# Optimization experiments

Hardware: AMD Instinct MI355X
Metric: run time of the kernel (lower is better)

The kernel has to match this reference:

```python
import jax, jax.numpy as jnp
import numpy as np

D_MODEL = 1024
N_HEADS = 16
D_HEAD = D_MODEL // N_HEADS
B, S = 2, 2048


def setup_inputs() -> dict:
    key = jax.random.key(0)
    ks = jax.random.split(key, 7)
    query = jax.random.normal(ks[0], (B, S, D_MODEL), dtype=jnp.float32)
    k_in = jax.random.normal(ks[1], (B, S, D_MODEL), dtype=jnp.float32)
    v_in = jax.random.normal(ks[2], (B, S, D_MODEL), dtype=jnp.float32)
    # causal mask: True = attend allowed (torch code keeps where mask != 0)
    mask = jnp.tril(jnp.ones((S, S), dtype=bool))
    scale = 1.0 / np.sqrt(D_MODEL)
    Wq = jax.random.normal(ks[3], (D_MODEL, D_MODEL), dtype=jnp.float32) * scale
    Wk = jax.random.normal(ks[4], (D_MODEL, D_MODEL), dtype=jnp.float32) * scale
    Wv = jax.random.normal(ks[5], (D_MODEL, D_MODEL), dtype=jnp.float32) * scale
    Wo = jax.random.normal(ks[6], (D_MODEL, D_MODEL), dtype=jnp.float32) * scale
    return {"query": query, "key": k_in, "value": v_in, "mask": mask,
            "Wq": Wq, "Wk": Wk, "Wv": Wv, "Wo": Wo}


def reference(query, key, value, mask, Wq, Wk, Wv, Wo):
    b, sq, d = query.shape
    # bias-free linear: x @ W.T (torch nn.Linear convention)
    q = (query @ Wq.T).reshape(b, sq, N_HEADS, D_HEAD).transpose(0, 2, 1, 3)  # b h s d
    k = (key @ Wk.T).reshape(b, -1, N_HEADS, D_HEAD).transpose(0, 2, 1, 3)
    v = (value @ Wv.T).reshape(b, -1, N_HEADS, D_HEAD).transpose(0, 2, 1, 3)
    scores = jnp.einsum('bhqd,bhkd->bhqk', q, k) / jnp.sqrt(jnp.float32(D_HEAD))
    scores = jnp.where(mask[None, None, :, :], scores, jnp.float32(-1e9))
    attn = jax.nn.softmax(scores, axis=-1)
    # dropout is identity in eval mode
    ctx = jnp.einsum('bhqk,bhkd->bhqd', attn, v)
    ctx = ctx.transpose(0, 2, 1, 3).reshape(b, sq, d)
    return ctx @ Wo.T
```

## Files before the change

### kernel.cpp

```cpp
#include <hip/hip_runtime.h>
#include <hip/hip_bf16.h>
#include <cstdint>


typedef unsigned short u16;
typedef u16 u16x4 __attribute__((ext_vector_type(4)));
typedef u16 u16x8 __attribute__((ext_vector_type(8)));
typedef unsigned u32x2 __attribute__((ext_vector_type(2)));
typedef unsigned u32x4 __attribute__((ext_vector_type(4)));
typedef __bf16 bf16x8 __attribute__((ext_vector_type(8)));
typedef float f32x4 __attribute__((ext_vector_type(4)));

#define S_LEN 2048
#define DM 1024
#define NH 16
#define DH 64
#define BATCH 2
#define MTOT (BATCH*S_LEN)

__device__ __forceinline__ u16 f2bf(float f) {
  union { float f; unsigned u; } v; v.f = f;
  unsigned r = v.u + 0x7FFFu + ((v.u >> 16) & 1u);
  return (u16)(r >> 16);
}

__device__ __forceinline__ f32x4 mfma16(u16x8 a, u16x8 b, f32x4 c) {
  return __builtin_amdgcn_mfma_f32_16x16x32_bf16(
      __builtin_bit_cast(bf16x8, a), __builtin_bit_cast(bf16x8, b), c, 0, 0, 0);
}
__device__ __forceinline__ unsigned cvtpk_bf16(float lo, float hi) {
  unsigned r;
  asm("v_cvt_pk_bf16_f32 %0, %1, %2" : "=v"(r) : "v"(lo), "v"(hi));
  return r;
}
__device__ __forceinline__ void gload16(const u16* g, u16* l) {
  __builtin_amdgcn_global_load_lds(
      (const __attribute__((address_space(1))) unsigned int*)g,
      (__attribute__((address_space(3))) unsigned int*)l, 16, 0, 0);
}

__global__ __launch_bounds__(256) void cvt_kernel(
    const float* __restrict__ s0, const float* __restrict__ s1,
    const float* __restrict__ s2, const float* __restrict__ s3,
    u16* __restrict__ d0, u16* __restrict__ d1,
    u16* __restrict__ d2, u16* __restrict__ d3) {
  const int y = blockIdx.y;
  const float* s = (y == 0) ? s0 : (y == 1) ? s1 : (y == 2) ? s2 : s3;
  u16* d       = (y == 0) ? d0 : (y == 1) ? d1 : (y == 2) ? d2 : d3;
  int i = (blockIdx.x * 256 + threadIdx.x) * 4;
  f32x4 v = *(const f32x4*)&s[i];
  u16x4 o;
  o[0] = f2bf(v[0]); o[1] = f2bf(v[1]); o[2] = f2bf(v[2]); o[3] = f2bf(v[3]);
  *(u16x4*)&d[i] = o;
}

#define BM 128
#define BN 128
#define BKK 32

template<int MODE, bool AF32>
__device__ __forceinline__ void gemm_core(const void* __restrict__ Av,
                                          const u16* __restrict__ Bw,
                                          void* __restrict__ Cv,
                                          int K, float scale,
                                          int bx, int by, u16* smem) {
  const int BUFSZ = AF32 ? 12288 : 8192;
  const int AOFF  = AF32 ? 8192  : 4096;
  const u16* A16 = (const u16*)Av;
  const float* A32 = (const float*)Av;
  const int tid  = threadIdx.x;
  const int lane = tid & 63, w = tid >> 6;
  const int g = lane >> 4, r16 = lane & 15;
  const int wm = w >> 1, wn = w & 1;
  const int rowBase = by * BM;
  const int colBase = bx * BN;
  f32x4 acc[4][4] = {};

  const int srowB = lane >> 2;
  const int skcB  = (lane & 3) * 8;
  const u16* gB[2]; int oB[2];
#pragma unroll
  for (int j = 0; j < 2; j++) {
    const int c = w * 2 + j;
    gB[j] = &Bw[(size_t)(colBase + c * 16 + srowB) * K + skcB];
    oB[j] = c * 512;
  }
  const u16* gA16[2]; int oA16[2];
  const float* gA32[4]; int oA32[4];
  if constexpr (AF32) {
    const int srow8 = lane >> 3;
    const int scF   = ((lane & 7) ^ srow8) * 4;
#pragma unroll
    for (int j = 0; j < 4; j++) {
      const int rb = w * 32 + j * 8;
      gA32[j] = &A32[(size_t)(rowBase + rb + srow8) * K + scF];
      oA32[j] = rb * 32;
    }
  } else {
#pragma unroll
    for (int j = 0; j < 2; j++) {
      const int c = w * 2 + j;
      gA16[j] = &A16[(size_t)(rowBase + c * 16 + srowB) * K + skcB];
      oA16[j] = c * 512;
    }
  }

  const int NT = K / BKK;
  {
    u16* base = smem;
    if constexpr (AF32) {
      float* a32 = (float*)base;
#pragma unroll
      for (int j = 0; j < 4; j++) gload16((const u16*)gA32[j], (u16*)(a32 + oA32[j]));
    } else {
#pragma unroll
      for (int j = 0; j < 2; j++) gload16(gA16[j], base + oA16[j]);
    }
#pragma unroll
    for (int j = 0; j < 2; j++) gload16(gB[j], base + AOFF + oB[j]);
  }
  int cur = 0;
  for (int t = 0; t < NT; ++t) {
    __syncthreads();
    if (t + 1 < NT) {
      const int k0 = (t + 1) * BKK;
      u16* base = smem + (cur ^ 1) * BUFSZ;
      if constexpr (AF32) {
        float* a32 = (float*)base;
#pragma unroll
        for (int j = 0; j < 4; j++) gload16((const u16*)(gA32[j] + k0), (u16*)(a32 + oA32[j]));
      } else {
#pragma unroll
        for (int j = 0; j < 2; j++) gload16(gA16[j] + k0, base + oA16[j]);
      }
#pragma unroll
      for (int j = 0; j < 2; j++) gload16(gB[j] + k0, base + AOFF + oB[j]);
    }
    u16* As = smem + cur * BUFSZ;
    u16* Bs = As + AOFF;
    float* As32 = (float*)As;
    u16x8 af[4], bfv[4];
    if constexpr (AF32) {
      const int rx = r16 & 7;
#pragma unroll
      for (int i = 0; i < 4; i++) {
        const int base_ = (wm * 64 + i * 16 + r16) * 32;
        f32x4 a0 = *(const f32x4*)&As32[base_ + (((g * 2)     ^ rx) * 4)];
        f32x4 a1 = *(const f32x4*)&As32[base_ + (((g * 2 + 1) ^ rx) * 4)];
        u32x4 wv = {cvtpk_bf16(a0[0], a0[1]), cvtpk_bf16(a0[2], a0[3]),
                    cvtpk_bf16(a1[0], a1[1]), cvtpk_bf16(a1[2], a1[3])};
        af[i] = __builtin_bit_cast(u16x8, wv);
      }
    } else {
#pragma unroll
      for (int i = 0; i < 4; i++)
        af[i] = *(const u16x8*)&As[(wm*64 + i*16 + r16) * BKK + g*8];
    }
#pragma unroll
    for (int j = 0; j < 4; j++) bfv[j] = *(const u16x8*)&Bs[(wn*64 + j*16 + r16) * BKK + g*8];
    __builtin_amdgcn_s_setprio(1);
#pragma unroll
    for (int i = 0; i < 4; i++)
#pragma unroll
      for (int j = 0; j < 4; j++) acc[i][j] = mfma16(af[i], bfv[j], acc[i][j]);
    __builtin_amdgcn_s_setprio(0);
    cur ^= 1;
  }
#pragma unroll
  for (int i = 0; i < 4; i++) {
#pragma unroll
    for (int j = 0; j < 4; j++) {
      int row = rowBase + wm*64 + i*16 + 4*g;
      int col = colBase + wn*64 + j*16 + r16;
      if (MODE == 0) {
        u16* O = (u16*)Cv;
        int head = col >> 6, d = col & 63;
#pragma unroll
        for (int r = 0; r < 4; r++)
          O[((size_t)head * MTOT + row + r) * DH + d] = f2bf(acc[i][j][r] * scale);
      } else if (MODE == 1) {
        u16x4 o;
#pragma unroll
        for (int r = 0; r < 4; r++) o[r] = f2bf(acc[i][j][r]);
        *(u16x4*)&((u16*)Cv)[(size_t)col * MTOT + row] = o;
      } else {
#pragma unroll
        for (int r = 0; r < 4; r++)
          ((float*)Cv)[(size_t)(row + r) * DM + col] = acc[i][j][r];
      }
    }
  }
}

__device__ __forceinline__ void gemm_remap(int& bx, int& by) {
  const int flat = blockIdx.x + 8 * blockIdx.y;
  const int xcd = flat & 7, i = flat >> 3;
  bx = i & 7;
  by = xcd * 4 + (i >> 3);
}

__global__ __launch_bounds__(256) void qkv_proj_kernel(
    const float* __restrict__ Xq, const float* __restrict__ Xk, const float* __restrict__ Xv,
    const u16* __restrict__ Wq, const u16* __restrict__ Wk, const u16* __restrict__ Wv,
    u16* __restrict__ Qp, u16* __restrict__ Kp, u16* __restrict__ Vt) {
  __shared__ u16 smem[24576];
  int bx, by; gemm_remap(bx, by);
  const int z = blockIdx.z;
  if (z == 0)      gemm_core<0, true>(Xq, Wq, Qp, DM, 0.125f * 1.44269504f, bx, by, smem);
  else if (z == 1) gemm_core<0, true>(Xk, Wk, Kp, DM, 1.0f, bx, by, smem);
  else             gemm_core<1, true>(Xv, Wv, Vt, DM, 1.0f, bx, by, smem);
}

__global__ __launch_bounds__(256) void out_proj_kernel(
    const u16* __restrict__ Ctx, const u16* __restrict__ Wo, float* __restrict__ Out) {
  __shared__ u16 smem[16384];
  int bx, by; gemm_remap(bx, by);
  gemm_core<2, false>(Ctx, Wo, Out, DM, 1.0f, bx, by, smem);
}


#define STAGE(B, T)                                                            \
  {                                                                            \
    const int kv0_ = (T) * 64;                                                 \
    _Pragma("unroll")                                                          \
    for (int j = 0; j < 2; j++) {                                              \
      const int rb = wv * 16 + j * 8;                                          \
      gload16(&Kbase[(size_t)(kv0_ + rb + srow) * DH + sc16 * 8],              \
              &Kl[B][rb * 64]);                                                \
      gload16(&Vbase[(size_t)(rb + srow) * MTOT + kv0_ + sc16 * 8],            \
              &Vl[B][rb * 64]);                                                \
    }                                                                          \
  }

#define TILE_BODY(BUF, T)                                                      \
  {                                                                            \
    const int kv0 = (T) * 64;                                                  \
    const f32x4 minit = {-16.f, -16.f, -16.f, -16.f};                          \
    f32x4 s[4] = {minit, minit, minit, minit};         \
    __builtin_amdgcn_s_setprio(1);                                             \
    _Pragma("unroll")                                                          \
    for (int f = 0; f < 4; f++) {                                              \
      _Pragma("unroll")                                                        \
      for (int ds = 0; ds < 2; ds++) {                                         \
        u16x8 kf = *(const u16x8*)&Kl[BUF][(f * 16 + q16) * 64 +               \
                                           ((ds * 4 + g) ^ qx7) * 8];          \
        s[f] = mfma16(kf, qf[ds], s[f]);                                       \
      }                                                                        \
    }                                                                          \
    __builtin_amdgcn_s_setprio(0);                                             \
    if ((T) == ntb - 1) {             \
      const int qg = qb16 + q16;                                               \
      _Pragma("unroll")                                                        \
      for (int f = 0; f < 4; f++)                                              \
        _Pragma("unroll")                                                      \
        for (int r = 0; r < 4; r++)                                            \
          if (kv0 + f * 16 + 4 * g + r > qg) s[f][r] = -1e30f;                 \
    }                                                                          \
    _Pragma("unroll")                                                          \
    for (int f = 0; f < 4; f++)                                                \
      _Pragma("unroll")                                                        \
      for (int r = 0; r < 4; r++) s[f][r] = exp2f(s[f][r]);                    \
            \
    _Pragma("unroll")                                                          \
    for (int f = 0; f < 4; f++) {                                              \
      const int cidx = (((2 * f + (g >> 1)) ^ qx7) * 8) + 4 * (g & 1);         \
      u32x2 pw = {cvtpk_bf16(s[f][0], s[f][1]), cvtpk_bf16(s[f][2], s[f][3])}; \
      *(u32x2*)&P16[q16 * 64 + cidx] = pw;                                     \
    }                                                                          \
    asm volatile("s_waitcnt lgkmcnt(0)" ::: "memory");                         \
    __builtin_amdgcn_sched_barrier(0);                                         \
    u16x8 pa0 = *(const u16x8*)&P16[q16 * 64 + ((g)     ^ qx7) * 8];           \
    u16x8 pa1 = *(const u16x8*)&P16[q16 * 64 + ((4 + g) ^ qx7) * 8];           \
    __builtin_amdgcn_s_setprio(1);                                             \
    lsum = mfma16(pa0, onesv, lsum);               \
    lsum = mfma16(pa1, onesv, lsum);                                           \
    _Pragma("unroll")                                                          \
    for (int dt = 0; dt < 4; dt++) {                                           \
      u16x8 vf0 = *(const u16x8*)&Vl[BUF][(dt * 16 + q16) * 64 +               \
                                          ((g)     ^ qx7) * 8];                \
      u16x8 vf1 = *(const u16x8*)&Vl[BUF][(dt * 16 + q16) * 64 +               \
                                          ((4 + g) ^ qx7) * 8];                \
      ctx[dt] = mfma16(pa0, vf0, ctx[dt]);                                     \
      ctx[dt] = mfma16(pa1, vf1, ctx[dt]);                                     \
    }                                                                          \
    __builtin_amdgcn_s_setprio(0);                                             \
  }

__global__ __launch_bounds__(256, 4) void attn_kernel(const u16* __restrict__ Qp,
                                                      const u16* __restrict__ Kp,
                                                      const u16* __restrict__ Vt,
                                                      u16* __restrict__ Ctx) {
  __shared__ u16 Kl[2][64 * 64];
  __shared__ u16 Vl[2][64 * 64];
  __shared__ u16 Pl[4][16 * 64];
  const int tid = threadIdx.x;
  const int lane = tid & 63, wv = tid >> 6;
  const int q16 = lane & 15, g = lane >> 4;
  const int qx7 = q16 & 7;
  const int flat = blockIdx.x;
  const int xcd = flat & 7, idx = flat >> 3;
  const int bh = xcd * 4 + (idx & 3);
  const int qc = 31 - (idx >> 2);
  const int bb = bh >> 4, h = bh & 15;
  const int qb16 = qc * 64 + wv * 16;

  const u16* Qbase = Qp + (size_t)(h * MTOT + bb * S_LEN) * DH;
  const u16* Kbase = Kp + (size_t)(h * MTOT + bb * S_LEN) * DH;
  const u16* Vbase = Vt + (size_t)(h * DH) * MTOT + bb * S_LEN;
  u16* P16 = Pl[wv];

  u16x8 qf[2];
#pragma unroll
  for (int ds = 0; ds < 2; ds++)
    qf[ds] = *(const u16x8*)&Qbase[(size_t)(qb16 + q16) * DH + ds * 32 + g * 8];

  f32x4 ctx[4] = {};
  f32x4 lsum = {};
  const u16x8 onesv = {0x3F80, 0x3F80, 0x3F80, 0x3F80,
                       0x3F80, 0x3F80, 0x3F80, 0x3F80};
  const int ntb = qc + 1;

  const int srow = lane >> 3;
  const int sc16 = (lane & 7) ^ srow;

  STAGE(0, 0);
  int cur = 0;
  for (int t = 0; t < ntb; ++t) {
    __syncthreads();
    if (t + 1 < ntb) STAGE(cur ^ 1, t + 1);
    TILE_BODY(cur, t);
    cur ^= 1;
  }

  float inv[4];
#pragma unroll
  for (int r = 0; r < 4; r++) inv[r] = 1.f / lsum[r];
#pragma unroll
  for (int dt = 0; dt < 4; dt++)
#pragma unroll
    for (int r = 0; r < 4; r++) {
      size_t grow = (size_t)(bb * S_LEN + qb16 + 4 * g + r) * DM + h * DH;
      Ctx[grow + dt * 16 + q16] = f2bf(ctx[dt][r] * inv[r]);
    }
}

extern "C" void kernel_launch(void* const* d_in, const int* in_sizes, int n_in,
                              void* d_out, int out_size, void* d_ws, size_t ws_size,
                              hipStream_t stream) {
  const float* q_in = (const float*)d_in[0];
  const float* k_in = (const float*)d_in[1];
  const float* v_in = (const float*)d_in[2];
  const float* wq = (const float*)d_in[4];
  const float* wk = (const float*)d_in[5];
  const float* wv = (const float*)d_in[6];
  const float* wo = (const float*)d_in[7];

  char* ws = (char*)d_ws;
  const size_t MB = 1024ull * 1024ull;
  u16* Qp  = (u16*)(ws + 0  * MB);
  u16* Kp  = (u16*)(ws + 8  * MB);
  u16* Vt  = (u16*)(ws + 16 * MB);
  u16* Ctx = (u16*)(ws + 24 * MB);
  u16* Wqb = (u16*)(ws + 56 * MB);
  u16* Wkb = (u16*)(ws + 58 * MB);
  u16* Wvb = (u16*)(ws + 60 * MB);
  u16* Wob = (u16*)(ws + 62 * MB);

  cvt_kernel<<<dim3(DM * DM / 1024, 4), 256, 0, stream>>>(
      wq, wk, wv, wo, Wqb, Wkb, Wvb, Wob);
  qkv_proj_kernel<<<dim3(8, MTOT / BM, 3), 256, 0, stream>>>(
      q_in, k_in, v_in, Wqb, Wkb, Wvb, Qp, Kp, Vt);
  attn_kernel<<<dim3(1024), 256, 0, stream>>>(Qp, Kp, Vt, Ctx);
  out_proj_kernel<<<dim3(8, MTOT / BM), 256, 0, stream>>>(Ctx, Wob, (float*)d_out);
}
```

Baseline: 108.1 us.

## Convert fp32 activations to bf16 in registers before staging to LDS

The fp32 A tile in the QKV projection is now loaded into registers, converted to bf16, and written to LDS after the MFMA block, replacing direct fp32 global-to-LDS copies and per-fragment conversion on every read. This halves LDS use for A (48KB to 32KB) and removes repeated conversions, and an XOR swizzle is added to A and B tiles to avoid bank conflicts. In exchange, the global loads now go through VGPRs, which raises register pressure and makes the prefetch depend on the register-write path.

```diff
diff --git a/kernel.cpp b/kernel.cpp
--- a/kernel.cpp
+++ b/kernel.cpp
@@ -7,7 +7,6 @@
 typedef u16 u16x4 __attribute__((ext_vector_type(4)));
 typedef u16 u16x8 __attribute__((ext_vector_type(8)));
 typedef unsigned u32x2 __attribute__((ext_vector_type(2)));
-typedef unsigned u32x4 __attribute__((ext_vector_type(4)));
 typedef __bf16 bf16x8 __attribute__((ext_vector_type(8)));
 typedef float f32x4 __attribute__((ext_vector_type(4)));
 
@@ -64,8 +63,6 @@
                                           void* __restrict__ Cv,
                                           int K, float scale,
                                           int bx, int by, u16* smem) {
-  const int BUFSZ = AF32 ? 12288 : 8192;
-  const int AOFF  = AF32 ? 8192  : 4096;
   const u16* A16 = (const u16*)Av;
   const float* A32 = (const float*)Av;
   const int tid  = threadIdx.x;
@@ -77,93 +74,92 @@
   f32x4 acc[4][4] = {};
 
   const int srowB = lane >> 2;
-  const int skcB  = (lane & 3) * 8;
+  const int swzB  = ((lane & 3) ^ ((lane >> 3) & 3)) * 8;
   const u16* gB[2]; int oB[2];
 #pragma unroll
   for (int j = 0; j < 2; j++) {
     const int c = w * 2 + j;
-    gB[j] = &Bw[(size_t)(colBase + c * 16 + srowB) * K + skcB];
+    gB[j] = &Bw[(size_t)(colBase + c * 16 + srowB) * K + swzB];
     oB[j] = c * 512;
   }
   const u16* gA16[2]; int oA16[2];
-  const float* gA32[4]; int oA32[4];
+  const float* gA32[4]; int oAw[4];
   if constexpr (AF32) {
-    const int srow8 = lane >> 3;
-    const int scF   = ((lane & 7) ^ srow8) * 4;
-#pragma unroll
-    for (int j = 0; j < 4; j++) {
-      const int rb = w * 32 + j * 8;
-      gA32[j] = &A32[(size_t)(rowBase + rb + srow8) * K + scF];
-      oA32[j] = rb * 32;
+    const int arow0 = tid >> 3;
+    const int ac4   = tid & 7;
+#pragma unroll
+    for (int p = 0; p < 4; p++) {
+      const int row = p * 32 + arow0;
+      gA32[p] = &A32[(size_t)(rowBase + row) * K + ac4 * 4];
+      oAw[p]  = row * 32 + (((ac4 >> 1) ^ ((row >> 1) & 3)) * 8) + (ac4 & 1) * 4;
     }
   } else {
 #pragma unroll
     for (int j = 0; j < 2; j++) {
       const int c = w * 2 + j;
-      gA16[j] = &A16[(size_t)(rowBase + c * 16 + srowB) * K + skcB];
+      gA16[j] = &A16[(size_t)(rowBase + c * 16 + srowB) * K + swzB];
       oA16[j] = c * 512;
     }
   }
 
   const int NT = K / BKK;
   {
-    u16* base = smem;
+#pragma unroll
+    for (int j = 0; j < 2; j++) gload16(gB[j], smem + 4096 + oB[j]);
     if constexpr (AF32) {
-      float* a32 = (float*)base;
-#pragma unroll
-      for (int j = 0; j < 4; j++) gload16((const u16*)gA32[j], (u16*)(a32 + oA32[j]));
+#pragma unroll
+      for (int p = 0; p < 4; p++) {
+        f32x4 av = *(const f32x4*)gA32[p];
+        u32x2 pw = {cvtpk_bf16(av[0], av[1]), cvtpk_bf16(av[2], av[3])};
+        *(u32x2*)&smem[oAw[p]] = pw;
+      }
     } else {
 #pragma unroll
-      for (int j = 0; j < 2; j++) gload16(gA16[j], base + oA16[j]);
-    }
-#pragma unroll
-    for (int j = 0; j < 2; j++) gload16(gB[j], base + AOFF + oB[j]);
-  }
+      for (int j = 0; j < 2; j++) gload16(gA16[j], smem + oA16[j]);
+    }
+  }
+  const int rswz = (r16 >> 1) & 3;
   int cur = 0;
   for (int t = 0; t < NT; ++t) {
     __syncthreads();
-    if (t + 1 < NT) {
-      const int k0 = (t + 1) * BKK;
-      u16* base = smem + (cur ^ 1) * BUFSZ;
+    f32x4 av[4];
+    const bool pf = (t + 1 < NT);
+    if (pf) {
+      const int k0n = (t + 1) * BKK;
+      u16* nbase = smem + (cur ^ 1) * 8192;
       if constexpr (AF32) {
-        float* a32 = (float*)base;
-#pragma unroll
-        for (int j = 0; j < 4; j++) gload16((const u16*)(gA32[j] + k0), (u16*)(a32 + oA32[j]));
+#pragma unroll
+        for (int p = 0; p < 4; p++) av[p] = *(const f32x4*)(gA32[p] + k0n);
       } else {
 #pragma unroll
-        for (int j = 0; j < 2; j++) gload16(gA16[j] + k0, base + oA16[j]);
+        for (int j = 0; j < 2; j++) gload16(gA16[j] + k0n, nbase + oA16[j]);
       }
 #pragma unroll
-      for (int j = 0; j < 2; j++) gload16(gB[j] + k0, base + AOFF + oB[j]);
-    }
-    u16* As = smem + cur * BUFSZ;
-    u16* Bs = As + AOFF;
-    float* As32 = (float*)As;
+      for (int j = 0; j < 2; j++) gload16(gB[j] + k0n, nbase + 4096 + oB[j]);
+    }
+    u16* As = smem + cur * 8192;
+    u16* Bs = As + 4096;
     u16x8 af[4], bfv[4];
-    if constexpr (AF32) {
-      const int rx = r16 & 7;
-#pragma unroll
-      for (int i = 0; i < 4; i++) {
-        const int base_ = (wm * 64 + i * 16 + r16) * 32;
-        f32x4 a0 = *(const f32x4*)&As32[base_ + (((g * 2)     ^ rx) * 4)];
-        f32x4 a1 = *(const f32x4*)&As32[base_ + (((g * 2 + 1) ^ rx) * 4)];
-        u32x4 wv = {cvtpk_bf16(a0[0], a0[1]), cvtpk_bf16(a0[2], a0[3]),
-                    cvtpk_bf16(a1[0], a1[1]), cvtpk_bf16(a1[2], a1[3])};
-        af[i] = __builtin_bit_cast(u16x8, wv);
-      }
-    } else {
-#pragma unroll
-      for (int i = 0; i < 4; i++)
-        af[i] = *(const u16x8*)&As[(wm*64 + i*16 + r16) * BKK + g*8];
-    }
-#pragma unroll
-    for (int j = 0; j < 4; j++) bfv[j] = *(const u16x8*)&Bs[(wn*64 + j*16 + r16) * BKK + g*8];
+#pragma unroll
+    for (int i = 0; i < 4; i++)
+      af[i]  = *(const u16x8*)&As[(wm*64 + i*16 + r16) * 32 + ((g ^ rswz) * 8)];
+#pragma unroll
+    for (int j = 0; j < 4; j++)
+      bfv[j] = *(const u16x8*)&Bs[(wn*64 + j*16 + r16) * 32 + ((g ^ rswz) * 8)];
     __builtin_amdgcn_s_setprio(1);
 #pragma unroll
     for (int i = 0; i < 4; i++)
 #pragma unroll
       for (int j = 0; j < 4; j++) acc[i][j] = mfma16(af[i], bfv[j], acc[i][j]);
     __builtin_amdgcn_s_setprio(0);
+    if (AF32 && pf) {
+      u16* nbase = smem + (cur ^ 1) * 8192;
+#pragma unroll
+      for (int p = 0; p < 4; p++) {
+        u32x2 pw = {cvtpk_bf16(av[p][0], av[p][1]), cvtpk_bf16(av[p][2], av[p][3])};
+        *(u32x2*)&nbase[oAw[p]] = pw;
+      }
+    }
     cur ^= 1;
   }
 #pragma unroll
@@ -203,7 +199,7 @@
     const float* __restrict__ Xq, const float* __restrict__ Xk, const float* __restrict__ Xv,
     const u16* __restrict__ Wq, const u16* __restrict__ Wk, const u16* __restrict__ Wv,
     u16* __restrict__ Qp, u16* __restrict__ Kp, u16* __restrict__ Vt) {
-  __shared__ u16 smem[24576];
+  __shared__ u16 smem[16384];
   int bx, by; gemm_remap(bx, by);
   const int z = blockIdx.z;
   if (z == 0)      gemm_core<0, true>(Xq, Wq, Qp, DM, 0.125f * 1.44269504f, bx, by, smem);
```

Result: slower. 117.2 us (+8.5%).
